# Optimization experiments

Hardware: AMD Instinct MI355X
Metric: run time of the kernel (lower is better)

Reference implementation:

```python
import jax, jax.numpy as jnp
import numpy as np

B, S, D, H = 2, 2048, 1024, 16
HD = D // H  # 64


def setup_inputs() -> dict:
    key = jax.random.key(0)
    ks = jax.random.split(key, 10)
    sc = 1.0 / np.sqrt(D)
    return {
        "decoder_hs": jax.random.normal(ks[0], (B, S, D), jnp.float32),
        "encoder_hs": jax.random.normal(ks[1], (B, S, D), jnp.float32),
        "Wq": jax.random.normal(ks[2], (D, D), jnp.float32) * sc,
        "bq": jax.random.normal(ks[3], (D,), jnp.float32) * 0.02,
        "Wk": jax.random.normal(ks[4], (D, D), jnp.float32) * sc,
        "bk": jax.random.normal(ks[5], (D,), jnp.float32) * 0.02,
        "Wv": jax.random.normal(ks[6], (D, D), jnp.float32) * sc,
        "bv": jax.random.normal(ks[7], (D,), jnp.float32) * 0.02,
        "Wp": jax.random.normal(ks[8], (D, D), jnp.float32) * sc,
        "bp": jax.random.normal(ks[9], (D,), jnp.float32) * 0.02,
    }


def reference(decoder_hs, encoder_hs, Wq, bq, Wk, bk, Wv, bv, Wp, bp):
    b, s, d = decoder_hs.shape
    # torch nn.Linear: y = x @ W.T + b, W is [out, in]
    q = decoder_hs @ Wq.T + bq
    k = encoder_hs @ Wk.T + bk
    v = encoder_hs @ Wv.T + bv
    # head split: [b, s, d] -> [b, h, s, hd]
    q = q.reshape(b, s, H, HD).transpose(0, 2, 1, 3)
    k = k.reshape(b, s, H, HD).transpose(0, 2, 1, 3)
    v = v.reshape(b, s, H, HD).transpose(0, 2, 1, 3)
    scale = 1.0 / np.sqrt(HD).astype(np.float32)
    att = jnp.einsum('bhqd,bhkd->bhqk', q, k) * scale
    att = jax.nn.softmax(att, axis=-1)
    y = jnp.einsum('bhqk,bhkd->bhqd', att, v)
    y = y.transpose(0, 2, 1, 3).reshape(b, s, d)
    return y @ Wp.T + bp
```

## Files before the change

kernel.cpp:

```cpp
#include <hip/hip_runtime.h>
#include <hip/hip_bf16.h>
#include <cstdint>
#include <cstddef>

#define BB 2
#define SS 2048
#define DD 1024
#define HH 16
#define HD 64

typedef __attribute__((ext_vector_type(8))) short bf16x8;
typedef __attribute__((ext_vector_type(4))) float f32x4;
typedef __attribute__((ext_vector_type(16))) float f32x16;

#define GLL(g, l) __builtin_amdgcn_global_load_lds( \
    (const __attribute__((address_space(1))) void*)(g), \
    (__attribute__((address_space(3))) void*)(l), 16, 0, 0)

__device__ __forceinline__ short f2bf_fast(float f) {
    uint32_t u = __float_as_uint(f);
    u += 0x7FFF + ((u >> 16) & 1);
    return (short)(u >> 16);
}
__device__ __forceinline__ uint32_t pack_bf2(float a, float b) {
    uint32_t ua = __float_as_uint(a), ub = __float_as_uint(b);
    ua += 0x7FFF + ((ua >> 16) & 1);
    ub += 0x7FFF + ((ub >> 16) & 1);
    return (ua >> 16) | (ub & 0xFFFF0000u);
}
__device__ __forceinline__ uint32_t cvtpk_bf2(float a, float b) {
    uint32_t r;
    asm("v_cvt_pk_bf16_f32 %0, %1, %2" : "=v"(r) : "v"(a), "v"(b));
    return r;
}
__device__ __forceinline__ void pl32swap(uint32_t& a, uint32_t& b) {
    asm("v_permlane32_swap_b32 %0, %1" : "+v"(a), "+v"(b));
}
__device__ __forceinline__ bf16x8 cvt8(const float* __restrict__ p) {
    float4 a = *(const float4*)p;
    float4 b = *(const float4*)(p + 4);
    union { uint32_t d[4]; bf16x8 v; } r;
    r.d[0] = pack_bf2(a.x, a.y);
    r.d[1] = pack_bf2(a.z, a.w);
    r.d[2] = pack_bf2(b.x, b.y);
    r.d[3] = pack_bf2(b.z, b.w);
    return r.v;
}

__global__ __launch_bounds__(256) void cvt6_kernel(
    const float* __restrict__ s0, const float* __restrict__ s1,
    const float* __restrict__ s2, const float* __restrict__ s3,
    const float* __restrict__ s4, const float* __restrict__ s5,
    short* __restrict__ d0, short* __restrict__ d1, short* __restrict__ d2,
    short* __restrict__ d3, short* __restrict__ d4, short* __restrict__ d5)
{
    const int id = blockIdx.x * 256 + threadIdx.x;
    const float* s; short* d; size_t off;
    if (id < 1048576) {
        int e = id >> 19;
        off = (size_t)(id & 524287) * 8;
        s = e ? s1 : s0;  d = e ? d1 : d0;
    } else {
        int j = id - 1048576;
        int w = j >> 17;
        off = (size_t)(j & 131071) * 8;
        s = (w == 0) ? s2 : (w == 1) ? s3 : (w == 2) ? s4 : s5;
        d = (w == 0) ? d2 : (w == 1) ? d3 : (w == 2) ? d4 : d5;
    }
    bf16x8 r = cvt8(s + off);
    *(uint4*)(d + off) = *(uint4*)&r;
}

template<int BF>
__global__ __launch_bounds__(256, 3) void qkv_gemm_kernel(
    const void* __restrict__ dec, const void* __restrict__ enc,
    const void* __restrict__ Wq, const void* __restrict__ Wk,
    const void* __restrict__ Wv,
    const float* __restrict__ bq, const float* __restrict__ bk,
    const float* __restrict__ bv,
    short* __restrict__ Qo, short* __restrict__ Ko, short* __restrict__ Vo)
{
    __shared__ short As[128 * 64];
    __shared__ short Bs[128 * 64];

    const int z = blockIdx.z;
    const void* Xv = (z == 0) ? dec : enc;
    const void* Wp_ = (z == 0) ? Wq : (z == 1) ? Wk : Wv;
    const float* bias = (z == 0) ? bq : (z == 1) ? bk : bv;
    short* Yo = (z == 0) ? Qo : (z == 1) ? Ko : Vo;
    const float qs = (z == 0) ? (0.125f * 1.44269504088896f) : 1.0f;

    const int t = threadIdx.x;
    const int lane = t & 63, wv = t >> 6;
    const int lr = lane & 15, quad = lane >> 4;
    const int e7 = lr & 7;
    const int wm = wv >> 1, wn = wv & 1;
    const int m0 = blockIdx.y * 128;
    const int n0 = blockIdx.x * 128;
    const int K = DD;

    f32x4 acc[4][4];
    #pragma unroll
    for (int i = 0; i < 4; i++)
        #pragma unroll
        for (int j = 0; j < 4; j++) acc[i][j] = (f32x4){0.f, 0.f, 0.f, 0.f};

    for (int kb = 0; kb < K; kb += 64) {
        __syncthreads();
        if (BF) {
            const short* Xb = (const short*)Xv;
            const short* Wb = (const short*)Wp_;
            #pragma unroll
            for (int c = 0; c < 4; c++) {
                int r0 = wv * 32 + c * 8;
                int r = r0 + (lane >> 3);
                int sc = ((lane & 7) ^ (r & 7)) * 8;
                GLL(Xb + (size_t)(m0 + r) * K + kb + sc, &As[r0 * 64]);
                GLL(Wb + (size_t)(n0 + r) * K + kb + sc, &Bs[r0 * 64]);
            }
        } else {
            const float* Xf = (const float*)Xv;
            const float* Wf = (const float*)Wp_;
            #pragma unroll
            for (int c = 0; c < 4; c++) {
                int id = t + c * 256;
                int r = id >> 3, lc = id & 7;
                int pc = (lc ^ (r & 7)) * 8;
                *(bf16x8*)&As[r * 64 + pc] = cvt8(Xf + (size_t)(m0 + r) * K + kb + lc * 8);
                *(bf16x8*)&Bs[r * 64 + pc] = cvt8(Wf + (size_t)(n0 + r) * K + kb + lc * 8);
            }
        }
        __syncthreads();

        bf16x8 af[4][2], bfr[4][2];
        #pragma unroll
        for (int kk = 0; kk < 2; kk++) {
            int pc = ((kk * 4 + quad) ^ e7) * 8;
            #pragma unroll
            for (int mi = 0; mi < 4; mi++)
                af[mi][kk] = *(const bf16x8*)&As[(wm * 64 + mi * 16 + lr) * 64 + pc];
            #pragma unroll
            for (int ni = 0; ni < 4; ni++)
                bfr[ni][kk] = *(const bf16x8*)&Bs[(wn * 64 + ni * 16 + lr) * 64 + pc];
        }
        #pragma unroll
        for (int kk = 0; kk < 2; kk++)
            #pragma unroll
            for (int mi = 0; mi < 4; mi++)
                #pragma unroll
                for (int ni = 0; ni < 4; ni++)
                    acc[mi][ni] = __builtin_amdgcn_mfma_f32_16x16x32_bf16(
                        af[mi][kk], bfr[ni][kk], acc[mi][ni], 0, 0, 0);
    }

    if (z < 2) {
        #pragma unroll
        for (int ni = 0; ni < 4; ni++) {
            int col = n0 + wn * 64 + ni * 16 + lr;
            int h = col >> 6, hd = col & 63;
            float bvv = bias[col];
            #pragma unroll
            for (int mi = 0; mi < 4; mi++) {
                #pragma unroll
                for (int r2 = 0; r2 < 4; r2++) {
                    int row = m0 + wm * 64 + mi * 16 + quad * 4 + r2;
                    int b = row >> 11, s = row & 2047;
                    float v = (acc[mi][ni][r2] + bvv) * qs;
                    size_t off = ((size_t)(b * HH + h) * SS + s) * HD + hd;
                    Yo[off] = f2bf_fast(v);
                }
            }
        }
    } else {
        #pragma unroll
        for (int ni = 0; ni < 4; ni++) {
            int col = n0 + wn * 64 + ni * 16 + lr;
            int h = col >> 6, hd = col & 63;
            float bvv = bias[col];
            #pragma unroll
            for (int mi = 0; mi < 4; mi++) {
                int s0 = m0 + wm * 64 + mi * 16 + quad * 4;
                int b = s0 >> 11, s = s0 & 2047;
                union { uint32_t d[2]; } u;
                u.d[0] = pack_bf2(acc[mi][ni][0] + bvv, acc[mi][ni][1] + bvv);
                u.d[1] = pack_bf2(acc[mi][ni][2] + bvv, acc[mi][ni][3] + bvv);
                size_t off = ((size_t)(b * HH + h) * HD + hd) * SS + s;
                *(uint2*)(Yo + off) = *(uint2*)&u;
            }
        }
    }
}

template<int WBF>
__global__ __launch_bounds__(256, 2) void proj_gemm_kernel(
    const short* __restrict__ X,
    const void* __restrict__ W, const float* __restrict__ bias,
    float* __restrict__ Y)
{
    __shared__ short As[64 * 32];
    __shared__ short Bs[128 * 32];

    const int t = threadIdx.x;
    const int lane = t & 63, wv = t >> 6;
    const int lr = lane & 15, quad = lane >> 4;
    const int wm = wv >> 1, wn = wv & 1;
    const int m0 = blockIdx.y * 64;
    const int n0 = blockIdx.x * 128;
    const int K = DD, N = DD;

    f32x4 acc[2][4];
    #pragma unroll
    for (int i = 0; i < 2; i++)
        #pragma unroll
        for (int j = 0; j < 4; j++) acc[i][j] = (f32x4){0.f, 0.f, 0.f, 0.f};

    for (int kb = 0; kb < K; kb += 32) {
        __syncthreads();
        {
            int r0 = wv * 16;
            int r = r0 + (lane >> 2), ch = (lane & 3) * 8;
            GLL(X + (size_t)(m0 + r) * K + kb + ch, &As[r0 * 32]);
        }
        if (WBF) {
            const short* Wb = (const short*)W;
            #pragma unroll
            for (int c = 0; c < 2; c++) {
                int r0 = wv * 32 + c * 16;
                int r = r0 + (lane >> 2), ch = (lane & 3) * 8;
                GLL(Wb + (size_t)(n0 + r) * K + kb + ch, &Bs[r0 * 32]);
            }
        } else {
            const float* Wf = (const float*)W;
            #pragma unroll
            for (int c = 0; c < 2; c++) {
                int id = t + c * 256;
                int r = id >> 2, c8 = (id & 3) * 8;
                *(bf16x8*)&Bs[r * 32 + c8] = cvt8(Wf + (size_t)(n0 + r) * K + kb + c8);
            }
        }
        __syncthreads();

        bf16x8 af[2], bfr[4];
        #pragma unroll
        for (int mi = 0; mi < 2; mi++)
            af[mi] = *(const bf16x8*)&As[(wm * 32 + mi * 16 + lr) * 32 + quad * 8];
        #pragma unroll
        for (int ni = 0; ni < 4; ni++)
            bfr[ni] = *(const bf16x8*)&Bs[(wn * 64 + ni * 16 + lr) * 32 + quad * 8];
        #pragma unroll
        for (int mi = 0; mi < 2; mi++)
            #pragma unroll
            for (int ni = 0; ni < 4; ni++)
                acc[mi][ni] = __builtin_amdgcn_mfma_f32_16x16x32_bf16(
                    af[mi], bfr[ni], acc[mi][ni], 0, 0, 0);
    }

    #pragma unroll
    for (int ni = 0; ni < 4; ni++) {
        int col = n0 + wn * 64 + ni * 16 + lr;
        float bvv = bias[col];
        #pragma unroll
        for (int mi = 0; mi < 2; mi++) {
            #pragma unroll
            for (int r2 = 0; r2 < 4; r2++) {
                int row = m0 + wm * 32 + mi * 16 + quad * 4 + r2;
                Y[(size_t)row * N + col] = acc[mi][ni][r2] + bvv;
            }
        }
    }
}

__global__ __launch_bounds__(256, 2) void attn_kernel(
    const short* __restrict__ Q,
    const short* __restrict__ Kgl,
    const short* __restrict__ Vt_g,
    short* __restrict__ Y)
{
    __shared__ short Ks[2][128][64];
    __shared__ short Vt[3][64][128];

    const int t = threadIdx.x;
    const int lane = t & 63, w = t >> 6;
    const int lq = lane & 31, hf = lane >> 5;
    const int gl = (lq & 7) ^ ((lq >> 3) & 3);

    const int bid = blockIdx.x;
    const int slot = bid >> 3;
    const int bh = ((slot >> 4) << 3) + (bid & 7);
    const int qt = slot & 15;
    const int b = bh >> 4, h = bh & 15;

    const int q = qt * 128 + w * 32 + lq;
    const short* Qp = Q + ((size_t)bh * SS + q) * HD;
    bf16x8 qf[4];
    #pragma unroll
    for (int j = 0; j < 4; j++)
        qf[j] = *(const bf16x8*)(Qp + j * 16 + hf * 8);

    f32x16 o[2];
    #pragma unroll
    for (int i = 0; i < 16; i++) { o[0][i] = 0.f; o[1][i] = 0.f; }
    f32x4 vsum = (f32x4){0.f, 0.f, 0.f, 0.f};

    const short* Kb = Kgl + (size_t)bh * SS * HD;
    const short* Vb = Vt_g + (size_t)bh * HD * SS;

    auto stage = [&](int kt1) {
        short* Kd = &Ks[kt1 & 1][0][0];
        short* Vd = &Vt[kt1 % 3][0][0];
        #pragma unroll
        for (int c = 0; c < 4; c++) {
            int r0 = w * 32 + c * 8;
            int r  = r0 + (lane >> 3);
            int g  = (r & 7) ^ ((r >> 3) & 3);
            int sc = ((lane & 7) ^ g) * 8;
            GLL(Kb + (size_t)(kt1 * 128 + r) * 64 + sc, Kd + r0 * 64);
        }
        #pragma unroll
        for (int c = 0; c < 4; c++) {
            int h0 = w * 16 + c * 4;
            int hd = h0 + (lane >> 4);
            int g  = (hd & 7) ^ ((hd >> 3) & 3);
            int s16 = (lane & 15) ^ g;
            GLL(Vb + (size_t)hd * SS + kt1 * 128 + s16 * 8, Vd + h0 * 128);
        }
    };

    auto qk = [&](int kt, f32x16 (&sc)[4]) {
        const short (*Kc)[64] = Ks[kt & 1];
        __builtin_amdgcn_s_setprio(1);
        #pragma unroll
        for (int j = 0; j < 4; j++)
            #pragma unroll
            for (int s = 0; s < 4; s++) {
                bf16x8 kf = *(const bf16x8*)&Kc[s * 32 + lq][((j * 2 + hf) ^ gl) * 8];
                sc[s] = __builtin_amdgcn_mfma_f32_32x32x16_bf16(kf, qf[j], sc[s], 0, 0, 0);
            }
        __builtin_amdgcn_s_setprio(0);
    };

    auto sm = [&](const f32x16& scs, bf16x8& p0, bf16x8& p1) {
        float ev[16];
        #pragma unroll
        for (int i = 0; i < 16; i++) ev[i] = __builtin_amdgcn_exp2f(scs[i]);
        #pragma unroll
        for (int r = 0; r < 4; r++)
            vsum += (f32x4){ev[4*r], ev[4*r+1], ev[4*r+2], ev[4*r+3]};
        uint32_t dw[8];
        #pragma unroll
        for (int i = 0; i < 8; i++) dw[i] = cvtpk_bf2(ev[2*i], ev[2*i+1]);
        pl32swap(dw[0], dw[2]); pl32swap(dw[1], dw[3]);
        pl32swap(dw[4], dw[6]); pl32swap(dw[5], dw[7]);
        union { uint32_t u[4]; bf16x8 v; } f0, f1;
        f0.u[0] = dw[0]; f0.u[1] = dw[1]; f0.u[2] = dw[2]; f0.u[3] = dw[3];
        f1.u[0] = dw[4]; f1.u[1] = dw[5]; f1.u[2] = dw[6]; f1.u[3] = dw[7];
        p0 = f0.v; p1 = f1.v;
    };

    auto pv4 = [&](const short* Vc, int s, bf16x8 p0, bf16x8 p1) {
        #pragma unroll
        for (int ds = 0; ds < 2; ds++) {
            const short* vrow = Vc + (ds * 32 + lq) * 128;
            bf16x8 va0 = *(const bf16x8*)&vrow[((s * 4 + 0 + hf) ^ gl) * 8];
            o[ds] = __builtin_amdgcn_mfma_f32_32x32x16_bf16(va0, p0, o[ds], 0, 0, 0);
            bf16x8 va1 = *(const bf16x8*)&vrow[((s * 4 + 2 + hf) ^ gl) * 8];
            o[ds] = __builtin_amdgcn_mfma_f32_32x32x16_bf16(va1, p1, o[ds], 0, 0, 0);
        }
    };

    bf16x8 pbA[4][2], pbB[4][2];

    auto body = [&](int kt, bf16x8 (&pbp)[4][2], bf16x8 (&pbc)[4][2]) {
        if (kt + 1 < 16) stage(kt + 1);
        f32x16 sc[4];
        #pragma unroll
        for (int s = 0; s < 4; s++)
            #pragma unroll
            for (int i = 0; i < 16; i++) sc[s][i] = 0.f;
        qk(kt, sc);
        __builtin_amdgcn_sched_barrier(0);
        const short* Vprev = &Vt[(kt + 2) % 3][0][0];
        __builtin_amdgcn_s_setprio(1);
        #pragma unroll
        for (int s = 0; s < 4; s++) {
            pv4(Vprev, s, pbp[s][0], pbp[s][1]);
            sm(sc[s], pbc[s][0], pbc[s][1]);
            __builtin_amdgcn_sched_group_barrier(0x100, 4, 0);
            __builtin_amdgcn_sched_group_barrier(0x008, 4, 0);
            __builtin_amdgcn_sched_group_barrier(0x001, 32, 0);
        }
        __builtin_amdgcn_s_setprio(0);
        __syncthreads();
    };

    stage(0);
    __syncthreads();

    {
        stage(1);
        f32x16 sc[4];
        #pragma unroll
        for (int s = 0; s < 4; s++)
            #pragma unroll
            for (int i = 0; i < 16; i++) sc[s][i] = 0.f;
        qk(0, sc);
        __builtin_amdgcn_sched_barrier(0);
        #pragma unroll
        for (int s = 0; s < 4; s++) sm(sc[s], pbA[s][0], pbA[s][1]);
        __syncthreads();
    }

    for (int kt = 1; kt <= 13; kt += 2) {
        body(kt, pbA, pbB);
        body(kt + 1, pbB, pbA);
    }
    body(15, pbA, pbB);

    __builtin_amdgcn_s_setprio(1);
    #pragma unroll
    for (int s = 0; s < 4; s++) pv4(&Vt[0][0][0], s, pbB[s][0], pbB[s][1]);
    __builtin_amdgcn_s_setprio(0);

    float lsum = (vsum[0] + vsum[1]) + (vsum[2] + vsum[3]);
    lsum += __shfl_xor(lsum, 32, 64);
    float inv = 1.0f / lsum;

    short* Yp = Y + ((size_t)b * SS + q) * DD + h * 64 + hf * 4;
    #pragma unroll
    for (int ds = 0; ds < 2; ds++)
        #pragma unroll
        for (int rr = 0; rr < 4; rr++) {
            union { uint32_t d[2]; } u;
            u.d[0] = pack_bf2(o[ds][rr*4+0] * inv, o[ds][rr*4+1] * inv);
            u.d[1] = pack_bf2(o[ds][rr*4+2] * inv, o[ds][rr*4+3] * inv);
            *(uint2*)(Yp + ds * 32 + rr * 8) = *(uint2*)&u;
        }
}

extern "C" void kernel_launch(void* const* d_in, const int* in_sizes, int n_in,
                              void* d_out, int out_size, void* d_ws, size_t ws_size,
                              hipStream_t stream) {
    const float* dec = (const float*)d_in[0];
    const float* enc = (const float*)d_in[1];
    const float* Wq  = (const float*)d_in[2];
    const float* bq  = (const float*)d_in[3];
    const float* Wk  = (const float*)d_in[4];
    const float* bk  = (const float*)d_in[5];
    const float* Wv  = (const float*)d_in[6];
    const float* bv  = (const float*)d_in[7];
    const float* Wp  = (const float*)d_in[8];
    const float* bp  = (const float*)d_in[9];

    const size_t per = (size_t)BB * HH * SS * HD;
    const size_t wsz = (size_t)DD * DD;
    short* ws = (short*)d_ws;
    short* Qb  = ws;
    short* Kb  = ws + per;
    short* Vtb = ws + 2 * per;
    short* Yb  = ws + 3 * per;

    dim3 qkv_grid(DD / 128, (BB * SS) / 128, 3);
    dim3 proj_grid(DD / 128, (BB * SS) / 64);
    const int attn_blocks = BB * HH * (SS / 128);
    const int cvt_blocks = (2 * 524288 + 4 * 131072) / 256;

    const size_t need = (6 * per + 4 * wsz) * sizeof(short);
    if (ws_size >= need) {
        short* decb = ws + 4 * per;
        short* encb = ws + 5 * per;
        short* Wqb  = ws + 6 * per;
        short* Wkb  = Wqb + wsz;
        short* Wvb  = Wqb + 2 * wsz;
        short* Wpb  = Wqb + 3 * wsz;
        cvt6_kernel<<<cvt_blocks, 256, 0, stream>>>(
            dec, enc, Wq, Wk, Wv, Wp, decb, encb, Wqb, Wkb, Wvb, Wpb);
        qkv_gemm_kernel<1><<<qkv_grid, 256, 0, stream>>>(
            decb, encb, Wqb, Wkb, Wvb, bq, bk, bv, Qb, Kb, Vtb);
        attn_kernel<<<attn_blocks, 256, 0, stream>>>(Qb, Kb, Vtb, Yb);
        proj_gemm_kernel<1><<<proj_grid, 256, 0, stream>>>(Yb, Wpb, bp, (float*)d_out);
    } else {
        qkv_gemm_kernel<0><<<qkv_grid, 256, 0, stream>>>(
            dec, enc, Wq, Wk, Wv, bq, bk, bv, Qb, Kb, Vtb);
        attn_kernel<<<attn_blocks, 256, 0, stream>>>(Qb, Kb, Vtb, Yb);
        proj_gemm_kernel<0><<<proj_grid, 256, 0, stream>>>(Yb, Wp, bp, (float*)d_out);
    }
}
```

Baseline: 194.6 us.

## Triple-buffer QKV GEMM shared tiles with async loads and single barrier per step

The QKV projection GEMM moves from a K=64 single-buffered loop with two barriers per step to a K=32 triple-buffered pipeline. Global-to-LDS loads for step k+2 are issued before computing step k, and vmcnt waits let loads overlap the MFMAs. MFMA sections also run at raised wave priority. In exchange, tiles lose the XOR swizzle, so the 64-byte row stride may cause LDS bank conflicts, and there are twice as many loop iterations.

```diff
diff --git a/kernel.cpp b/kernel.cpp
--- a/kernel.cpp
+++ b/kernel.cpp
@@ -80,8 +80,8 @@
     const float* __restrict__ bv,
     short* __restrict__ Qo, short* __restrict__ Ko, short* __restrict__ Vo)
 {
-    __shared__ short As[128 * 64];
-    __shared__ short Bs[128 * 64];
+    __shared__ short As3[3][128 * 32];
+    __shared__ short Bs3[3][128 * 32];
 
     const int z = blockIdx.z;
     const void* Xv = (z == 0) ? dec : enc;
@@ -93,7 +93,6 @@
     const int t = threadIdx.x;
     const int lane = t & 63, wv = t >> 6;
     const int lr = lane & 15, quad = lane >> 4;
-    const int e7 = lr & 7;
     const int wm = wv >> 1, wn = wv & 1;
     const int m0 = blockIdx.y * 128;
     const int n0 = blockIdx.x * 128;
@@ -105,52 +104,88 @@
         #pragma unroll
         for (int j = 0; j < 4; j++) acc[i][j] = (f32x4){0.f, 0.f, 0.f, 0.f};
 
-    for (int kb = 0; kb < K; kb += 64) {
-        __syncthreads();
-        if (BF) {
-            const short* Xb = (const short*)Xv;
-            const short* Wb = (const short*)Wp_;
-            #pragma unroll
-            for (int c = 0; c < 4; c++) {
-                int r0 = wv * 32 + c * 8;
-                int r = r0 + (lane >> 3);
-                int sc = ((lane & 7) ^ (r & 7)) * 8;
-                GLL(Xb + (size_t)(m0 + r) * K + kb + sc, &As[r0 * 64]);
-                GLL(Wb + (size_t)(n0 + r) * K + kb + sc, &Bs[r0 * 64]);
-            }
-        } else {
-            const float* Xf = (const float*)Xv;
-            const float* Wf = (const float*)Wp_;
-            #pragma unroll
-            for (int c = 0; c < 4; c++) {
-                int id = t + c * 256;
-                int r = id >> 3, lc = id & 7;
-                int pc = (lc ^ (r & 7)) * 8;
-                *(bf16x8*)&As[r * 64 + pc] = cvt8(Xf + (size_t)(m0 + r) * K + kb + lc * 8);
-                *(bf16x8*)&Bs[r * 64 + pc] = cvt8(Wf + (size_t)(n0 + r) * K + kb + lc * 8);
-            }
-        }
-        __syncthreads();
-
-        bf16x8 af[4][2], bfr[4][2];
-        #pragma unroll
-        for (int kk = 0; kk < 2; kk++) {
-            int pc = ((kk * 4 + quad) ^ e7) * 8;
+    if (BF) {
+        const short* Xb = (const short*)Xv;
+        const short* Wb = (const short*)Wp_;
+        auto stage = [&](int kb, short* Ab, short* Bb) {
+            #pragma unroll
+            for (int c = 0; c < 2; c++) {
+                int r0 = wv * 32 + c * 16;
+                int r = r0 + (lane >> 2), ch = (lane & 3) * 8;
+                GLL(Xb + (size_t)(m0 + r) * K + kb + ch, Ab + r0 * 32);
+                GLL(Wb + (size_t)(n0 + r) * K + kb + ch, Bb + r0 * 32);
+            }
+        };
+
+        short *a0 = &As3[0][0], *a1 = &As3[1][0], *a2 = &As3[2][0];
+        short *b0 = &Bs3[0][0], *b1 = &Bs3[1][0], *b2 = &Bs3[2][0];
+
+        stage(0, a0, b0);
+        stage(32, a1, b1);
+        asm volatile("s_waitcnt vmcnt(4)" ::: "memory");
+        __builtin_amdgcn_s_barrier();
+        asm volatile("" ::: "memory");
+
+        for (int kt = 0; kt < 32; kt++) {
+            if (kt < 30) stage((kt + 2) * 32, a2, b2);
+
+            bf16x8 af[4], bfr[4];
             #pragma unroll
             for (int mi = 0; mi < 4; mi++)
-                af[mi][kk] = *(const bf16x8*)&As[(wm * 64 + mi * 16 + lr) * 64 + pc];
+                af[mi] = *(const bf16x8*)&a0[(wm * 64 + mi * 16 + lr) * 32 + quad * 8];
             #pragma unroll
             for (int ni = 0; ni < 4; ni++)
-                bfr[ni][kk] = *(const bf16x8*)&Bs[(wn * 64 + ni * 16 + lr) * 64 + pc];
-        }
-        #pragma unroll
-        for (int kk = 0; kk < 2; kk++)
+                bfr[ni] = *(const bf16x8*)&b0[(wn * 64 + ni * 16 + lr) * 32 + quad * 8];
+
+            __builtin_amdgcn_s_setprio(1);
             #pragma unroll
             for (int mi = 0; mi < 4; mi++)
                 #pragma unroll
                 for (int ni = 0; ni < 4; ni++)
                     acc[mi][ni] = __builtin_amdgcn_mfma_f32_16x16x32_bf16(
-                        af[mi][kk], bfr[ni][kk], acc[mi][ni], 0, 0, 0);
+                        af[mi], bfr[ni], acc[mi][ni], 0, 0, 0);
+            __builtin_amdgcn_s_setprio(0);
+
+            if (kt < 30) {
+                asm volatile("s_waitcnt vmcnt(4)" ::: "memory");
+                __builtin_amdgcn_s_barrier();
+                asm volatile("" ::: "memory");
+            } else if (kt == 30) {
+                asm volatile("s_waitcnt vmcnt(0)" ::: "memory");
+                __builtin_amdgcn_s_barrier();
+                asm volatile("" ::: "memory");
+            }
+            short* tp = a0; a0 = a1; a1 = a2; a2 = tp;
+            tp = b0; b0 = b1; b1 = b2; b2 = tp;
+        }
+    } else {
+        const float* Xf = (const float*)Xv;
+        const float* Wf = (const float*)Wp_;
+        for (int kb = 0; kb < K; kb += 32) {
+            __syncthreads();
+            #pragma unroll
+            for (int c = 0; c < 2; c++) {
+                int id = t + c * 256;
+                int r = id >> 2, c8 = (id & 3) * 8;
+                *(bf16x8*)&As3[0][r * 32 + c8] = cvt8(Xf + (size_t)(m0 + r) * K + kb + c8);
+                *(bf16x8*)&Bs3[0][r * 32 + c8] = cvt8(Wf + (size_t)(n0 + r) * K + kb + c8);
+            }
+            __syncthreads();
+
+            bf16x8 af[4], bfr[4];
+            #pragma unroll
+            for (int mi = 0; mi < 4; mi++)
+                af[mi] = *(const bf16x8*)&As3[0][(wm * 64 + mi * 16 + lr) * 32 + quad * 8];
+            #pragma unroll
+            for (int ni = 0; ni < 4; ni++)
+                bfr[ni] = *(const bf16x8*)&Bs3[0][(wn * 64 + ni * 16 + lr) * 32 + quad * 8];
+            #pragma unroll
+            for (int mi = 0; mi < 4; mi++)
+                #pragma unroll
+                for (int ni = 0; ni < 4; ni++)
+                    acc[mi][ni] = __builtin_amdgcn_mfma_f32_16x16x32_bf16(
+                        af[mi], bfr[ni], acc[mi][ni], 0, 0, 0);
+        }
     }
 
     if (z < 2) {
```

After: 200.3 us. +2.9%, slower.
